# Kernel tuning notes

Measured on AMD Instinct MI355X. Metric: run time of the kernel, lower is better.

The kernel has to match this reference:

```python
import jax, jax.numpy as jnp
import numpy as np
from jax import lax

K_GROUPS = 4
CH = 256
CG = CH // K_GROUPS  # 64
KK = 9  # 3x3 kernel taps


def setup_inputs() -> dict:
    key = jax.random.key(0)
    ks = jax.random.split(key, 4)
    x = jax.random.normal(ks[0], (16, CH, 64, 64), dtype=jnp.float32)
    # offset-predicting conv: Cg -> 18 (2 offsets per 3x3 tap); small init so offsets are modest
    off_w = jax.random.normal(ks[1], (K_GROUPS, 18, CG, 3, 3), dtype=jnp.float32) * 0.01
    off_b = jnp.zeros((K_GROUPS, 18), dtype=jnp.float32)
    # deformable conv weights: Cg -> Cg, 3x3
    def_w = jax.random.normal(ks[2], (K_GROUPS, CG, CG, 3, 3), dtype=jnp.float32) * (1.0 / np.sqrt(CG * KK))
    def_b = jnp.zeros((K_GROUPS, CG), dtype=jnp.float32)
    return {"x": x, "off_w": off_w, "off_b": off_b, "def_w": def_w, "def_b": def_b}


def _bilinear_sample(img, py, px):
    # img: [B,Cg,H,W]; py,px: [B,KK,H,W] float sample coords -> [B,Cg,KK,H,W]
    B, C, H, W = img.shape
    K = py.shape[1]
    imgf = img.reshape(B, C, H * W)
    y0 = jnp.floor(py)
    x0 = jnp.floor(px)
    wy = py - y0
    wx = px - x0

    def gather(yi, xi, wgt):
        valid = (yi >= 0) & (yi < H) & (xi >= 0) & (xi < W)  # zero padding outside
        yc = jnp.clip(yi, 0, H - 1).astype(jnp.int32)
        xc = jnp.clip(xi, 0, W - 1).astype(jnp.int32)
        idx = (yc * W + xc).reshape(B, 1, K * H * W)
        v = jnp.take_along_axis(imgf, idx, axis=2).reshape(B, C, K, H, W)
        w = (wgt * valid.astype(img.dtype)).reshape(B, 1, K, H, W)
        return v * w

    return (gather(y0, x0, (1 - wy) * (1 - wx))
            + gather(y0, x0 + 1, (1 - wy) * wx)
            + gather(y0 + 1, x0, wy * (1 - wx))
            + gather(y0 + 1, x0 + 1, wy * wx))


def _group_forward(xg, ow, ob, dw, db):
    # xg: [B,Cg,H,W]
    B, C, H, W = xg.shape
    offset = lax.conv_general_dilated(xg, ow, (1, 1), ((1, 1), (1, 1)),
                                      dimension_numbers=("NCHW", "OIHW", "NCHW"))
    offset = offset + ob[None, :, None, None]            # [B,18,H,W]
    off = offset.reshape(B, KK, 2, H, W)                  # per-tap (dy,dx)
    ky, kx = jnp.meshgrid(jnp.arange(-1, 2), jnp.arange(-1, 2), indexing="ij")
    ky = ky.reshape(KK).astype(xg.dtype)
    kx = kx.reshape(KK).astype(xg.dtype)
    hh = jnp.arange(H, dtype=xg.dtype)
    ww = jnp.arange(W, dtype=xg.dtype)
    py = off[:, :, 0] + ky[None, :, None, None] + hh[None, None, :, None]  # [B,KK,H,W]
    px = off[:, :, 1] + kx[None, :, None, None] + ww[None, None, None, :]
    sampled = _bilinear_sample(xg, py, px)                # [B,Cg,KK,H,W]
    out = jnp.einsum("oik,bikhw->bohw", dw.reshape(dw.shape[0], dw.shape[1], KK), sampled)
    return out + db[None, :, None, None]


def reference(x, off_w, off_b, def_w, def_b):
    xs = jnp.split(x, K_GROUPS, axis=1)  # mirrors torch.split over channel groups
    outs = [_group_forward(xs[g], off_w[g], off_b[g], def_w[g], def_b[g])
            for g in range(K_GROUPS)]
    return jnp.concatenate(outs, axis=1)
```

## Files before the change

kernel.cpp:

```cpp
#include <hip/hip_runtime.h>
#include <hip/hip_bf16.h>
#include <hip/hip_fp16.h>

#define B_  16
#define G_  4
#define CG  64
#define H_  64
#define W_  64
#define KK  9
#define HW  (H_ * W_)
#define IP  72
#define PD  68
#define XSLICE (PD * PD * CG)

typedef short    short8  __attribute__((ext_vector_type(8)));
typedef _Float16 half8   __attribute__((ext_vector_type(8)));
typedef _Float16 h2      __attribute__((ext_vector_type(2)));
typedef float    f32x4   __attribute__((ext_vector_type(4)));
typedef float    f32x16  __attribute__((ext_vector_type(16)));

__device__ __forceinline__ short f2h(float v) {
    _Float16 h = (_Float16)v;
    short s;
    __builtin_memcpy(&s, &h, 2);
    return s;
}

__device__ __forceinline__ unsigned int pk2h(float a, float b) {
    h2 h = { (_Float16)a, (_Float16)b };
    unsigned int u;
    __builtin_memcpy(&u, &h, 4);
    return u;
}

__device__ __forceinline__ unsigned int interp2h(unsigned int c00, unsigned int c01,
                                                 unsigned int c10, unsigned int c11,
                                                 h2 w00, h2 w01, h2 w10, h2 w11) {
    h2 v00, v01, v10, v11;
    __builtin_memcpy(&v00, &c00, 4);
    __builtin_memcpy(&v01, &c01, 4);
    __builtin_memcpy(&v10, &c10, 4);
    __builtin_memcpy(&v11, &c11, 4);
    h2 r = v00 * w00 + v01 * w01 + v10 * w10 + v11 * w11;
    unsigned int o;
    __builtin_memcpy(&o, &r, 4);
    return o;
}

__global__ __launch_bounds__(256)
void prep_all(const float* __restrict__ x,
              const float* __restrict__ off_w,
              const float* __restrict__ def_w,
              short* __restrict__ xTpad,
              short* __restrict__ dwA32,
              short* __restrict__ owA)
{
    const int blk = blockIdx.x;
    const int t   = threadIdx.x;

    if (blk < 1024) {
        const int bg = blk >> 4;
        const int y0 = (blk & 15) * 4;

        __shared__ unsigned int sBw[4 * CG * 33];

        const float* src = x + (size_t)bg * CG * HW + (size_t)y0 * W_;
        const int i  = t >> 2;
        const int x0 = (t & 3) * 16;

        float4 v[4][4];
#pragma unroll
        for (int r = 0; r < 4; r++) {
            const float* sp = src + (size_t)i * HW + r * W_ + x0;
#pragma unroll
            for (int c = 0; c < 4; c++) v[r][c] = ((const float4*)sp)[c];
        }

#pragma unroll
        for (int r = 0; r < 4; r++) {
#pragma unroll
            for (int c = 0; c < 4; c++) {
                const unsigned int u0 = pk2h(v[r][c].x, v[r][c].y);
                const unsigned int u1 = pk2h(v[r][c].z, v[r][c].w);
                const int base = (r * CG + i) * 33 + ((x0 + 4 * c) >> 1);
                sBw[base]     = u0;
                sBw[base + 1] = u1;
            }
        }
        __syncthreads();

        const short* sBs = (const short*)sBw;
        short* dst = xTpad + (size_t)bg * XSLICE;
#pragma unroll
        for (int r = 0; r < 4; r++) {
            const int yp = y0 + 2 + r;
            for (int task = t; task < PD * 8; task += 256) {
                const int ich = task & 7;
                const int xp  = task >> 3;
                const int xx  = xp - 2;
                short8 o = {0, 0, 0, 0, 0, 0, 0, 0};
                if ((unsigned)xx < (unsigned)W_) {
#pragma unroll
                    for (int e = 0; e < 8; e++)
                        o[e] = sBs[(r * CG + ich * 8 + e) * 66 + xx];
                }
                *(short8*)(dst + ((size_t)yp * PD + xp) * CG + ich * 8) = o;
            }
        }
        return;
    }

    if (blk < 1088) {
        const int bg = blk - 1024;
        short* dstb = xTpad + (size_t)bg * XSLICE;
        const int4 z = {0, 0, 0, 0};
        int4* d0 = (int4*)(dstb);
        int4* d1 = (int4*)(dstb + (size_t)66 * PD * CG);
        const int n16 = (2 * PD * CG * 2) / 16;
        for (int c = t; c < n16; c += 256) { d0[c] = z; d1[c] = z; }
        return;
    }

    const int tid = (blk - 1088) * 256 + t;
    const int ndw = G_ * KK * 4096;
    const int now = G_ * 18 * 2 * 4 * 16 * 8;
    if (tid < ndw) {
        const int e    = tid & 7;
        const int o    = (tid >> 3) & 31;
        const int q2   = (tid >> 8) & 1;
        const int step = (tid >> 9) & 3;
        const int mt   = (tid >> 11) & 1;
        const int gk   = tid >> 12;
        const int k    = gk % KK;
        const int g    = gk / KK;
        const int oo   = mt * 32 + o;
        const int i    = step * 16 + q2 * 8 + e;
        dwA32[tid] = f2h(def_w[((g * CG + oo) * CG + i) * KK + k]);
    } else if (tid < ndw + now) {
        const int t2 = tid - ndw;
        const int e  = t2 & 7;
        const int jj = (t2 >> 3) & 15;
        const int q  = (t2 >> 7) & 3;
        const int tm = (t2 >> 9) & 1;
        const int gs = t2 >> 10;
        const int s  = gs % 18;
        const int g  = gs / 18;
        const int j  = tm * 16 + jj;
        const int rc = s >> 1;
        const int i  = (s & 1) * 32 + q * 8 + e;
        owA[t2] = (j < 18) ? f2h(off_w[((g * 18 + j) * CG + i) * KK + rc]) : (short)0;
    }
}

__global__ __launch_bounds__(256, 4)
void deform_main(const short* __restrict__ xTpad,
                 const float* __restrict__ off_b,
                 const float* __restrict__ def_b,
                 const short* __restrict__ dwA32,
                 const short* __restrict__ owA,
                 float* __restrict__ out)
{
    const int raw = blockIdx.x;
    const int r8  = raw & 7;
    const int h   = (raw >> 3) & 63;
    const int q8  = raw >> 9;
    const int bg  = q8 * 8 + r8;
    const int b   = bg >> 2;
    const int g   = bg & 3;

    __shared__ float2 pcs[KK][64];
    __shared__ short  sT[2][64 * IP];

    const int t    = threadIdx.x;
    const int lane = t & 63;
    const int p    = t >> 6;
    const int nn   = lane & 15;
    const int q    = lane >> 4;

    const short* xb = xTpad + (size_t)bg * XSLICE;

    {
        const short* owAg = owA + g * 18 * 1024;
        f32x4 oa0 = {0.f, 0.f, 0.f, 0.f};
        f32x4 oa1 = {0.f, 0.f, 0.f, 0.f};
#pragma unroll
        for (int rc = 0; rc < 9; rc++) {
            const int rr = rc / 3;
            const int cc = rc % 3;
            const short* cp = xb + ((h + rr + 1) * PD + (p * 16 + nn + cc + 1)) * CG + q * 8;
            const half8 b0 = *(const half8*)cp;
            const half8 b1 = *(const half8*)(cp + 32);
            const int s0 = rc * 2, s1 = rc * 2 + 1;
            const half8 a00 = *(const half8*)(owAg + ((s0 * 2 + 0) * 4 + q) * 128 + nn * 8);
            const half8 a01 = *(const half8*)(owAg + ((s0 * 2 + 1) * 4 + q) * 128 + nn * 8);
            const half8 a10 = *(const half8*)(owAg + ((s1 * 2 + 0) * 4 + q) * 128 + nn * 8);
            const half8 a11 = *(const half8*)(owAg + ((s1 * 2 + 1) * 4 + q) * 128 + nn * 8);
            oa0 = __builtin_amdgcn_mfma_f32_16x16x32_f16(a00, b0, oa0, 0, 0, 0);
            oa1 = __builtin_amdgcn_mfma_f32_16x16x32_f16(a01, b0, oa1, 0, 0, 0);
            oa0 = __builtin_amdgcn_mfma_f32_16x16x32_f16(a10, b1, oa0, 0, 0, 0);
            oa1 = __builtin_amdgcn_mfma_f32_16x16x32_f16(a11, b1, oa1, 0, 0, 0);
        }
        const int n = p * 16 + nn;
#pragma unroll
        for (int reg = 0; reg < 4; reg++) {
            const int j  = q * 4 + reg;
            const int kk = j >> 1;
            const float v = oa0[reg] + off_b[g * 18 + j];
            if ((j & 1) == 0) pcs[kk][n].x = v + (float)(kk / 3) + (float)(h + 1);
            else              pcs[kk][n].y = v + (float)(kk % 3) + (float)(n + 1);
        }
        if (q == 0) {
            pcs[8][n].x = oa1[0] + off_b[g * 18 + 16] + 2.0f + (float)(h + 1);
            pcs[8][n].y = oa1[1] + off_b[g * 18 + 17] + 2.0f + (float)(n + 1);
        }
    }

    const int mt  = p >> 1;
    const int nt  = p & 1;
    const int n31 = lane & 31;
    const int q2  = lane >> 5;

    f32x16 acc = {0.f};
    const short* dwg = dwA32 + g * KK * 4096;

    const int posL  = lane >> 3;
    const int chidx = lane & 7;
    const int posA  = p * 16 + posL;
    const int posB  = posA + 8;

    uint4 ca00, ca01, ca10, ca11;
    uint4 cb00, cb01, cb10, cb11;
    float wya, wxa, wyb, wxb;

    auto issue_g = [&](int k) {
        {
            const float2 pc = pcs[k][posA];
            const float yf = floorf(pc.x);
            const float xf = floorf(pc.y);
            wya = pc.x - yf;
            wxa = pc.y - xf;
            int y0 = (int)yf;
            int x0 = (int)xf;
            y0 = (y0 < 0) ? 0 : ((y0 > 66) ? 66 : y0);
            x0 = (x0 < 0) ? 0 : ((x0 > 66) ? 66 : x0);
            const short* cp = xb + (y0 * PD + x0) * CG + chidx * 8;
            ca00 = *(const uint4*)cp;
            ca01 = *(const uint4*)(cp + CG);
            ca10 = *(const uint4*)(cp + PD * CG);
            ca11 = *(const uint4*)(cp + PD * CG + CG);
        }
        {
            const float2 pc = pcs[k][posB];
            const float yf = floorf(pc.x);
            const float xf = floorf(pc.y);
            wyb = pc.x - yf;
            wxb = pc.y - xf;
            int y0 = (int)yf;
            int x0 = (int)xf;
            y0 = (y0 < 0) ? 0 : ((y0 > 66) ? 66 : y0);
            x0 = (x0 < 0) ? 0 : ((x0 > 66) ? 66 : x0);
            const short* cp = xb + (y0 * PD + x0) * CG + chidx * 8;
            cb00 = *(const uint4*)cp;
            cb01 = *(const uint4*)(cp + CG);
            cb10 = *(const uint4*)(cp + PD * CG);
            cb11 = *(const uint4*)(cp + PD * CG + CG);
        }
    };

    auto write_t = [&](short* __restrict__ sTb) {
        {
            const float a00 = (1.0f - wya) * (1.0f - wxa);
            const float a01 = (1.0f - wya) * wxa;
            const float a10 = wya * (1.0f - wxa);
            const float a11 = wya * wxa;
            const h2 w00 = { (_Float16)a00, (_Float16)a00 };
            const h2 w01 = { (_Float16)a01, (_Float16)a01 };
            const h2 w10 = { (_Float16)a10, (_Float16)a10 };
            const h2 w11 = { (_Float16)a11, (_Float16)a11 };
            uint4 ov;
            ov.x = interp2h(ca00.x, ca01.x, ca10.x, ca11.x, w00, w01, w10, w11);
            ov.y = interp2h(ca00.y, ca01.y, ca10.y, ca11.y, w00, w01, w10, w11);
            ov.z = interp2h(ca00.z, ca01.z, ca10.z, ca11.z, w00, w01, w10, w11);
            ov.w = interp2h(ca00.w, ca01.w, ca10.w, ca11.w, w00, w01, w10, w11);
            *(uint4*)&sTb[posA * IP + chidx * 8] = ov;
        }
        {
            const float a00 = (1.0f - wyb) * (1.0f - wxb);
            const float a01 = (1.0f - wyb) * wxb;
            const float a10 = wyb * (1.0f - wxb);
            const float a11 = wyb * wxb;
            const h2 w00 = { (_Float16)a00, (_Float16)a00 };
            const h2 w01 = { (_Float16)a01, (_Float16)a01 };
            const h2 w10 = { (_Float16)a10, (_Float16)a10 };
            const h2 w11 = { (_Float16)a11, (_Float16)a11 };
            uint4 ov;
            ov.x = interp2h(cb00.x, cb01.x, cb10.x, cb11.x, w00, w01, w10, w11);
            ov.y = interp2h(cb00.y, cb01.y, cb10.y, cb11.y, w00, w01, w10, w11);
            ov.z = interp2h(cb00.z, cb01.z, cb10.z, cb11.z, w00, w01, w10, w11);
            ov.w = interp2h(cb00.w, cb01.w, cb10.w, cb11.w, w00, w01, w10, w11);
            *(uint4*)&sTb[posB * IP + chidx * 8] = ov;
        }
    };

    auto einsum_t = [&](int k, const short* __restrict__ sTb) {
        const short* dwk = dwg + k * 4096;
        const half8 af0 = *(const half8*)(dwk + ((mt * 4 + 0) * 2 + q2) * 256 + n31 * 8);
        const half8 af1 = *(const half8*)(dwk + ((mt * 4 + 1) * 2 + q2) * 256 + n31 * 8);
        const half8 af2 = *(const half8*)(dwk + ((mt * 4 + 2) * 2 + q2) * 256 + n31 * 8);
        const half8 af3 = *(const half8*)(dwk + ((mt * 4 + 3) * 2 + q2) * 256 + n31 * 8);
        const half8 bf0 = *(const half8*)&sTb[(nt * 32 + n31) * IP + 0 * 16 + q2 * 8];
        const half8 bf1 = *(const half8*)&sTb[(nt * 32 + n31) * IP + 1 * 16 + q2 * 8];
        const half8 bf2 = *(const half8*)&sTb[(nt * 32 + n31) * IP + 2 * 16 + q2 * 8];
        const half8 bf3 = *(const half8*)&sTb[(nt * 32 + n31) * IP + 3 * 16 + q2 * 8];
        acc = __builtin_amdgcn_mfma_f32_32x32x16_f16(af0, bf0, acc, 0, 0, 0);
        acc = __builtin_amdgcn_mfma_f32_32x32x16_f16(af1, bf1, acc, 0, 0, 0);
        acc = __builtin_amdgcn_mfma_f32_32x32x16_f16(af2, bf2, acc, 0, 0, 0);
        acc = __builtin_amdgcn_mfma_f32_32x32x16_f16(af3, bf3, acc, 0, 0, 0);
    };

    issue_g(0);
    write_t(&sT[0][0]);
    __syncthreads();
#pragma unroll
    for (int k = 0; k < KK; k++) {
        if (k < KK - 1) issue_g(k + 1);
        einsum_t(k, &sT[k & 1][0]);
        if (k < KK - 1) write_t(&sT[(k + 1) & 1][0]);
        __syncthreads();
    }

    float* outb = out + (size_t)(b * 256 + g * 64) * HW + h * W_;
    const int n = nt * 32 + n31;
#pragma unroll
    for (int reg = 0; reg < 16; reg++) {
        const int o = mt * 32 + (reg & 3) + 8 * (reg >> 2) + 4 * q2;
        outb[(size_t)o * HW + n] = acc[reg] + def_b[g * 64 + o];
    }
}

__global__ __launch_bounds__(256, 4)
void deform_fallback(const float* __restrict__ x,
                     const float* __restrict__ off_w,
                     const float* __restrict__ off_b,
                     const float* __restrict__ def_w,
                     const float* __restrict__ def_b,
                     float* __restrict__ out)
{
    const int raw = blockIdx.x;
    const int r8  = raw & 7;
    const int h   = (raw >> 3) & 63;
    const int q8  = raw >> 9;
    const int bg  = q8 * 8 + r8;
    const int b   = bg >> 2;
    const int g   = bg & 3;

    __shared__ float pys[KK][W_];
    __shared__ float pxs[KK][W_];
    __shared__ float buf[8192];
    float* red   = buf;
    float* s_lds = buf;
    float* dwTl  = buf + 4096;

    const int t = threadIdx.x;
    const int w = t & 63;
    const int p = t >> 6;

    const float* xg = x + (size_t)(b * 256 + g * 64) * HW;

    float acc[18];
#pragma unroll
    for (int j = 0; j < 18; j++) acc[j] = 0.0f;
    {
        const int i0 = p * 16;
        for (int ii = 0; ii < 16; ii++) {
            const int i = i0 + ii;
            const float* xi = xg + i * HW;
#pragma unroll
            for (int r = 0; r < 3; r++) {
                const int y = h + r - 1;
                if ((unsigned)y >= (unsigned)H_) continue;
#pragma unroll
                for (int c = 0; c < 3; c++) {
                    const int xc = w + c - 1;
                    const float xv = ((unsigned)xc < (unsigned)W_) ? xi[y * W_ + xc] : 0.0f;
#pragma unroll
                    for (int j = 0; j < 18; j++) {
                        const float wv = off_w[((g * 18 + j) * CG + i) * 9 + r * 3 + c];
                        acc[j] = fmaf(wv, xv, acc[j]);
                    }
                }
            }
        }
    }
#pragma unroll
    for (int j = 0; j < 18; j++) red[(p * 18 + j) * 64 + w] = acc[j];
    __syncthreads();
    for (int idx = t; idx < 18 * 64; idx += 256) {
        const int j  = idx >> 6;
        const int ww = idx & 63;
        float v = red[(0 * 18 + j) * 64 + ww] + red[(1 * 18 + j) * 64 + ww]
                + red[(2 * 18 + j) * 64 + ww] + red[(3 * 18 + j) * 64 + ww];
        v += off_b[g * 18 + j];
        const int k = j >> 1;
        if ((j & 1) == 0) pys[k][ww] = v + (float)(k / 3 - 1) + (float)h;
        else              pxs[k][ww] = v + (float)(k % 3 - 1) + (float)ww;
    }
    __syncthreads();

    float facc[16];
#pragma unroll
    for (int qd = 0; qd < 16; qd++) facc[qd] = 0.0f;
    const int w4 = (t & 15) << 2;
    const int o4 = (t >> 4) << 2;

    for (int k = 0; k < KK; k++) {
#pragma unroll
        for (int n = 0; n < 16; n++) {
            const int v = t + 256 * n;
            const int i = v >> 6;
            const int o = v & 63;
            dwTl[v] = def_w[((g * CG + o) * CG + i) * KK + k];
        }
        const float py  = pys[k][w];
        const float px  = pxs[k][w];
        const float y0f = floorf(py);
        const float x0f = floorf(px);
        const float wy  = py - y0f;
        const float wx  = px - x0f;
        const int   y0  = (int)y0f;
        const int   x0  = (int)x0f;
        const float w00 = (1.0f - wy) * (1.0f - wx);
        const float w01 = (1.0f - wy) * wx;
        const float w10 = wy * (1.0f - wx);
        const float w11 = wy * wx;
        const bool vy0 = (unsigned)y0       < (unsigned)H_;
        const bool vy1 = (unsigned)(y0 + 1) < (unsigned)H_;
        const bool vx0 = (unsigned)x0       < (unsigned)W_;
        const bool vx1 = (unsigned)(x0 + 1) < (unsigned)W_;
        const int a00 = y0 * W_ + x0;
#pragma unroll
        for (int n = 0; n < 16; n++) {
            const int i = (n << 2) + p;
            const float* xi = xg + i * HW;
            const float v00 = (vy0 && vx0) ? xi[a00]          : 0.0f;
            const float v01 = (vy0 && vx1) ? xi[a00 + 1]      : 0.0f;
            const float v10 = (vy1 && vx0) ? xi[a00 + W_]     : 0.0f;
            const float v11 = (vy1 && vx1) ? xi[a00 + W_ + 1] : 0.0f;
            s_lds[i * 64 + w] = w00 * v00 + w01 * v01 + w10 * v10 + w11 * v11;
        }
        __syncthreads();
#pragma unroll 4
        for (int i = 0; i < CG; i++) {
            const float4 sv = *(const float4*)&s_lds[i * 64 + w4];
            const float4 dv = *(const float4*)&dwTl[i * 64 + o4];
            facc[0]  = fmaf(dv.x, sv.x, facc[0]);
            facc[1]  = fmaf(dv.x, sv.y, facc[1]);
            facc[2]  = fmaf(dv.x, sv.z, facc[2]);
            facc[3]  = fmaf(dv.x, sv.w, facc[3]);
            facc[4]  = fmaf(dv.y, sv.x, facc[4]);
            facc[5]  = fmaf(dv.y, sv.y, facc[5]);
            facc[6]  = fmaf(dv.y, sv.z, facc[6]);
            facc[7]  = fmaf(dv.y, sv.w, facc[7]);
            facc[8]  = fmaf(dv.z, sv.x, facc[8]);
            facc[9]  = fmaf(dv.z, sv.y, facc[9]);
            facc[10] = fmaf(dv.z, sv.z, facc[10]);
            facc[11] = fmaf(dv.z, sv.w, facc[11]);
            facc[12] = fmaf(dv.w, sv.x, facc[12]);
            facc[13] = fmaf(dv.w, sv.y, facc[13]);
            facc[14] = fmaf(dv.w, sv.z, facc[14]);
            facc[15] = fmaf(dv.w, sv.w, facc[15]);
        }
        __syncthreads();
    }

    float* outp = out + (size_t)(b * 256 + g * 64) * HW + h * W_;
#pragma unroll
    for (int oo = 0; oo < 4; oo++) {
        const int o = o4 + oo;
        const float bias = def_b[g * 64 + o];
        float4 r;
        r.x = facc[oo * 4 + 0] + bias;
        r.y = facc[oo * 4 + 1] + bias;
        r.z = facc[oo * 4 + 2] + bias;
        r.w = facc[oo * 4 + 3] + bias;
        *(float4*)&outp[o * HW + w4] = r;
    }
}

extern "C" void kernel_launch(void* const* d_in, const int* in_sizes, int n_in,
                              void* d_out, int out_size, void* d_ws, size_t ws_size,
                              hipStream_t stream)
{
    (void)in_sizes; (void)n_in; (void)out_size;
    const float* x     = (const float*)d_in[0];
    const float* off_w = (const float*)d_in[1];
    const float* off_b = (const float*)d_in[2];
    const float* def_w = (const float*)d_in[3];
    const float* def_b = (const float*)d_in[4];
    float* out = (float*)d_out;

    const size_t xT_bytes  = (size_t)B_ * G_ * XSLICE * 2;
    const size_t dw_bytes  = (size_t)G_ * KK * 4096 * 2;
    const size_t ow_bytes  = (size_t)G_ * 18 * 1024 * 2;
    const size_t need = xT_bytes + dw_bytes + ow_bytes;

    const int nblk   = B_ * G_ * H_;
    const int nprepw = (G_ * KK * 4096 + G_ * 18 * 1024 + 255) / 256;
    const int nprep  = 1024 + 64 + nprepw;

    if (ws_size >= need) {
        short* xTpad = (short*)d_ws;
        short* dwA32 = (short*)((char*)d_ws + xT_bytes);
        short* owA   = (short*)((char*)d_ws + xT_bytes + dw_bytes);
        prep_all<<<nprep, 256, 0, stream>>>(x, off_w, def_w, xTpad, dwA32, owA);
        deform_main<<<nblk, 256, 0, stream>>>(xTpad, off_b, def_b, dwA32, owA, out);
    } else {
        deform_fallback<<<nblk, 256, 0, stream>>>(x, off_w, off_b, def_w, def_b, out);
    }
}
```

Measured before the change: 219.2 us.

## Stage conv weights through double-buffered LDS and vectorize output stores via LDS transpose

Offset-conv weights and the deformable-conv weight tiles are now copied cooperatively into double-buffered shared memory, one 16-byte chunk per thread, before the MFMA fragments read them. Previously each wave fetched its fragments straight from global memory. The epilogue also writes the accumulators to an LDS scratch tile and then emits coalesced float4 stores, replacing the scattered per-element stores. The cost is an extra 16 KB of LDS, which may reduce occupancy, plus a barrier in every iteration of the offset-conv loop.

Result: faster. 208.6 us (-4.8%).

```diff
diff --git a/kernel.cpp b/kernel.cpp
--- a/kernel.cpp
+++ b/kernel.cpp
@@ -170,6 +170,7 @@
 
     __shared__ float2 pcs[KK][64];
     __shared__ short  sT[2][64 * IP];
+    __shared__ short  sW[2][4096];
 
     const int t    = threadIdx.x;
     const int lane = t & 63;
@@ -183,22 +184,29 @@
         const short* owAg = owA + g * 18 * 1024;
         f32x4 oa0 = {0.f, 0.f, 0.f, 0.f};
         f32x4 oa1 = {0.f, 0.f, 0.f, 0.f};
+
+        *(uint4*)&sW[0][(0 & 1) * 2048 + t * 8] = *(const uint4*)(owAg + t * 8);
+        __syncthreads();
 #pragma unroll
         for (int rc = 0; rc < 9; rc++) {
             const int rr = rc / 3;
             const int cc = rc % 3;
+            if (rc < 8)
+                *(uint4*)&sW[0][((rc + 1) & 1) * 2048 + t * 8] =
+                    *(const uint4*)(owAg + (rc + 1) * 2048 + t * 8);
             const short* cp = xb + ((h + rr + 1) * PD + (p * 16 + nn + cc + 1)) * CG + q * 8;
             const half8 b0 = *(const half8*)cp;
             const half8 b1 = *(const half8*)(cp + 32);
-            const int s0 = rc * 2, s1 = rc * 2 + 1;
-            const half8 a00 = *(const half8*)(owAg + ((s0 * 2 + 0) * 4 + q) * 128 + nn * 8);
-            const half8 a01 = *(const half8*)(owAg + ((s0 * 2 + 1) * 4 + q) * 128 + nn * 8);
-            const half8 a10 = *(const half8*)(owAg + ((s1 * 2 + 0) * 4 + q) * 128 + nn * 8);
-            const half8 a11 = *(const half8*)(owAg + ((s1 * 2 + 1) * 4 + q) * 128 + nn * 8);
+            const short* aw = &sW[0][(rc & 1) * 2048];
+            const half8 a00 = *(const half8*)(aw +        q * 128 + nn * 8);
+            const half8 a01 = *(const half8*)(aw +  512 + q * 128 + nn * 8);
+            const half8 a10 = *(const half8*)(aw + 1024 + q * 128 + nn * 8);
+            const half8 a11 = *(const half8*)(aw + 1536 + q * 128 + nn * 8);
             oa0 = __builtin_amdgcn_mfma_f32_16x16x32_f16(a00, b0, oa0, 0, 0, 0);
             oa1 = __builtin_amdgcn_mfma_f32_16x16x32_f16(a01, b0, oa1, 0, 0, 0);
             oa0 = __builtin_amdgcn_mfma_f32_16x16x32_f16(a10, b1, oa0, 0, 0, 0);
             oa1 = __builtin_amdgcn_mfma_f32_16x16x32_f16(a11, b1, oa1, 0, 0, 0);
+            __syncthreads();
         }
         const int n = p * 16 + nn;
 #pragma unroll
@@ -302,12 +310,17 @@
         }
     };
 
-    auto einsum_t = [&](int k, const short* __restrict__ sTb) {
+    auto stage_af = [&](int k, short* __restrict__ sWb) {
         const short* dwk = dwg + k * 4096;
-        const half8 af0 = *(const half8*)(dwk + ((mt * 4 + 0) * 2 + q2) * 256 + n31 * 8);
-        const half8 af1 = *(const half8*)(dwk + ((mt * 4 + 1) * 2 + q2) * 256 + n31 * 8);
-        const half8 af2 = *(const half8*)(dwk + ((mt * 4 + 2) * 2 + q2) * 256 + n31 * 8);
-        const half8 af3 = *(const half8*)(dwk + ((mt * 4 + 3) * 2 + q2) * 256 + n31 * 8);
+        *(uint4*)&sWb[t * 8]        = *(const uint4*)(dwk + t * 8);
+        *(uint4*)&sWb[2048 + t * 8] = *(const uint4*)(dwk + 2048 + t * 8);
+    };
+
+    auto einsum_t = [&](const short* __restrict__ sTb, const short* __restrict__ sWb) {
+        const half8 af0 = *(const half8*)&sWb[((mt * 4 + 0) * 2 + q2) * 256 + n31 * 8];
+        const half8 af1 = *(const half8*)&sWb[((mt * 4 + 1) * 2 + q2) * 256 + n31 * 8];
+        const half8 af2 = *(const half8*)&sWb[((mt * 4 + 2) * 2 + q2) * 256 + n31 * 8];
+        const half8 af3 = *(const half8*)&sWb[((mt * 4 + 3) * 2 + q2) * 256 + n31 * 8];
         const half8 bf0 = *(const half8*)&sTb[(nt * 32 + n31) * IP + 0 * 16 + q2 * 8];
         const half8 bf1 = *(const half8*)&sTb[(nt * 32 + n31) * IP + 1 * 16 + q2 * 8];
         const half8 bf2 = *(const half8*)&sTb[(nt * 32 + n31) * IP + 2 * 16 + q2 * 8];
@@ -318,23 +331,46 @@
         acc = __builtin_amdgcn_mfma_f32_32x32x16_f16(af3, bf3, acc, 0, 0, 0);
     };
 
+    stage_af(0, &sW[1][0]);
     issue_g(0);
     write_t(&sT[0][0]);
     __syncthreads();
 #pragma unroll
     for (int k = 0; k < KK; k++) {
-        if (k < KK - 1) issue_g(k + 1);
-        einsum_t(k, &sT[k & 1][0]);
+        if (k < KK - 1) {
+            issue_g(k + 1);
+            stage_af(k + 1, &sW[k & 1][0]);
+        }
+        einsum_t(&sT[k & 1][0], &sW[(k + 1) & 1][0]);
         if (k < KK - 1) write_t(&sT[(k + 1) & 1][0]);
         __syncthreads();
     }
 
-    float* outb = out + (size_t)(b * 256 + g * 64) * HW + h * W_;
-    const int n = nt * 32 + n31;
-#pragma unroll
-    for (int reg = 0; reg < 16; reg++) {
-        const int o = mt * 32 + (reg & 3) + 8 * (reg >> 2) + 4 * q2;
-        outb[(size_t)o * HW + n] = acc[reg] + def_b[g * 64 + o];
+    float* eT = (float*)&sT[0][0];
+    {
+        const int n = nt * 32 + n31;
+#pragma unroll
+        for (int reg = 0; reg < 16; reg++) {
+            const int o = mt * 32 + (reg & 3) + 8 * (reg >> 2) + 4 * q2;
+            eT[o * 65 + n] = acc[reg];
+        }
+    }
+    __syncthreads();
+    {
+        const int o    = t & 63;
+        const int part = t >> 6;
+        const float bias = def_b[g * 64 + o];
+        float* outp = out + (size_t)(b * 256 + g * 64) * HW + h * W_ + (size_t)o * HW + part * 16;
+        const float* e = &eT[o * 65 + part * 16];
+#pragma unroll
+        for (int j0 = 0; j0 < 4; j0++) {
+            float4 r;
+            r.x = e[j0 * 4 + 0] + bias;
+            r.y = e[j0 * 4 + 1] + bias;
+            r.z = e[j0 * 4 + 2] + bias;
+            r.w = e[j0 * 4 + 3] + bias;
+            *(float4*)&outp[j0 * 4] = r;
+        }
     }
 }
 
```
